# Performance work log

Measured on AMD Instinct MI355X. Metric: run time of the kernel, lower is better.

## Reference

```python
import jax, jax.numpy as jnp
import numpy as np

LMAX = 2
C = 128            # uniform multiplicity per degree
H = 128            # hidden channels
M = (LMAX + 1) ** 2  # 9 spherical coefficients
EPS = 1e-6


def _pack_indices():
    # flat layout per degree block: [mul, 2l+1] channel-major; packed layout: [coeff, channel]
    pack = np.zeros(M * C, dtype=np.int64)
    offset = 0
    for l in range(LMAX + 1):
        dim = 2 * l + 1
        for m in range(dim):
            coeff = l * l + m
            for c in range(C):
                pack[coeff * C + c] = offset + c * dim + m
        offset += C * dim
    unpack = np.argsort(pack)
    return jnp.asarray(pack), jnp.asarray(unpack)

PACK_IDX, UNPACK_IDX = _pack_indices()
# expand_index: degree index for each of the M coefficients
EXPAND_IDX = jnp.asarray(np.repeat(np.arange(LMAX + 1), 2 * np.arange(LMAX + 1) + 1))


def setup_inputs() -> dict:
    key = jax.random.key(0)
    ks = jax.random.split(key, 6)
    N = 10000
    A = 42  # (2*(lmax+1)) * (2*(lmax+1)+1) = 6*7 flattened S2 grid points
    bound = 1.0 / np.sqrt(C)
    return {
        "x": jax.random.normal(ks[0], (N, M * C), dtype=jnp.float32),
        "norm_weight": jnp.ones((LMAX + 1, C), dtype=jnp.float32),
        "w1": jax.random.uniform(ks[1], (LMAX + 1, H, C), jnp.float32, -bound, bound),
        "b1": jnp.zeros((1, 1, H), dtype=jnp.float32),
        "grid_w": jax.random.uniform(ks[2], (2 * H, H), jnp.float32, -bound, bound),
        "grid_b": jnp.zeros((2 * H,), dtype=jnp.float32),
        "w2": jax.random.uniform(ks[3], (LMAX + 1, C, H), jnp.float32, -bound, bound),
        "b2": jnp.zeros((1, 1, C), dtype=jnp.float32),
        "to_grid_mat": jax.random.normal(ks[4], (A, M), dtype=jnp.float32) * 0.3,
        "from_grid_mat": jax.random.normal(ks[5], (M, A), dtype=jnp.float32) * 0.3,
    }


def reference(x, norm_weight, w1, b1, grid_w, grid_b, w2, b2, to_grid_mat, from_grid_mat):
    N = x.shape[0]
    # --- pack flat irreps -> [N, M, C] (pure permutation gather; no padding for uniform irreps)
    p = jnp.take(x, PACK_IDX, axis=1).reshape(N, M, C)
    # --- merged equivariant RMS norm over all (coeff, channel), per-degree-channel affine
    rms = jnp.sqrt(jnp.mean(p * p, axis=(1, 2), keepdims=True) + EPS)
    h = (p / rms) * norm_weight[EXPAND_IDX][None]  # [N, M, C]
    # --- SO3LinearFlat #1: per-degree dense C -> H, bias only on l=0 coeff
    h = jnp.einsum("nmc,mhc->nmh", h, w1[EXPAND_IDX])
    h = h.at[:, 0:1, :].add(b1)
    # --- to S2 grid: [N, M, H] -> [N, A, H]
    g = jnp.einsum("am,nmh->nah", to_grid_mat, h)
    # --- pointwise SwiGLU on grid: H -> 2H linear, silu gate
    z = jnp.einsum("nah,oh->nao", g, grid_w) + grid_b
    g = jax.nn.silu(z[..., :H]) * z[..., H:]
    # --- from S2 grid: [N, A, H] -> [N, M, H]
    h = jnp.einsum("ma,nah->nmh", from_grid_mat, g)
    # --- SO3LinearFlat #2: per-degree dense H -> C, bias only on l=0 coeff
    out = jnp.einsum("nmh,mch->nmc", h, w2[EXPAND_IDX])
    out = out.at[:, 0:1, :].add(b2)
    # --- unpack back to flat irreps layout
    return jnp.take(out.reshape(N, M * C), UNPACK_IDX, axis=1)
```

## Files before the change

kernel.cpp:

```cpp
#include <hip/hip_runtime.h>
#include <math.h>

typedef unsigned short u16;
typedef __attribute__((ext_vector_type(8))) short bf16x8;
typedef __attribute__((ext_vector_type(4))) float f32x4;
typedef __attribute__((ext_vector_type(16))) float f32x16;

constexpr int OFF_W1 = 0;
constexpr int OFF_W2 = 49152;
constexpr int OFF_GW = 98304;
constexpr int OFF_TG = 131072;
constexpr int OFF_FG = 132096;
constexpr int WS_ELEMS = 134144;

__device__ __forceinline__ u16 f2bf(float f) {
    unsigned u = __float_as_uint(f);
    u += 0x7FFFu + ((u >> 16) & 1u);
    return (u16)(u >> 16);
}

__global__ void prep_kernel(const float* __restrict__ w1, const float* __restrict__ gw,
                            const float* __restrict__ w2, const float* __restrict__ tg,
                            const float* __restrict__ fg, u16* __restrict__ wsb) {
    const int idx = blockIdx.x * blockDim.x + threadIdx.x;
    const int str = gridDim.x * blockDim.x;
    for (int i = idx; i < 49152; i += str) wsb[OFF_W1 + i] = f2bf(w1[i]);
    for (int i = idx; i < 49152; i += str) wsb[OFF_W2 + i] = f2bf(w2[i]);
    for (int i = idx; i < 32768; i += str) wsb[OFF_GW + i] = f2bf(gw[i]);
    for (int i = idx; i < 1024; i += str) {
        int a = i >> 4, k = i & 15;
        wsb[OFF_TG + i] = (a < 42 && k < 9) ? f2bf(tg[a * 9 + k]) : (u16)0;
    }
    for (int i = idx; i < 2048; i += str) {
        int m = i >> 6, k = i & 63;
        wsb[OFF_FG + i] = (m < 9 && k < 42) ? f2bf(fg[m * 42 + k]) : (u16)0;
    }
}

__global__ __launch_bounds__(256, 2) void eqffn_mfma(
    const float* __restrict__ x, const float* __restrict__ nw,
    const float* __restrict__ b1f, const float* __restrict__ gbf,
    const float* __restrict__ b2f, const u16* __restrict__ wsb,
    float* __restrict__ out, int N)
{
    __shared__ u16 sh_a1[64 * 136];
    __shared__ u16 sh_h1T[4 * 128 * 16];
    __shared__ u16 sh_g[48 * 136];
    __shared__ u16 sh_g2T[128 * 72];
    __shared__ float sh_nw[384];
    __shared__ float sh_b1[128];
    __shared__ float sh_b2[128];
    __shared__ float sh_gb[256];

    const int tid  = threadIdx.x;
    const int w    = tid >> 6;
    const int lane = tid & 63;
    const int q    = lane >> 4;
    const int r    = lane & 15;
    const int r32  = lane & 31;
    const int half = lane >> 5;
    const int n0   = blockIdx.x * 4;

    for (int i = tid; i < 384; i += 256) sh_nw[i] = nw[i];
    if (tid < 128) { sh_b1[tid] = b1f[tid]; sh_b2[tid] = b2f[tid]; }
    sh_gb[tid] = gbf[tid];
    {
        unsigned long long* z1 = (unsigned long long*)sh_h1T;
        for (int i = tid; i < 2048; i += 256) z1[i] = 0ull;
        unsigned long long* z2 = (unsigned long long*)sh_g2T;
        for (int i = tid; i < 2304; i += 256) z2[i] = 0ull;
    }
    __syncthreads();

    const int myn = n0 + w;
    float4 xv[5];
    float ss = 0.f;
    if (myn < N) {
        const float4* xr = (const float4*)(x + (size_t)myn * 1152);
        for (int i = lane, c2 = 0; i < 288; i += 64, ++c2) {
            float4 v = xr[i]; xv[c2] = v;
            ss += v.x * v.x + v.y * v.y + v.z * v.z + v.w * v.w;
        }
    }
    #pragma unroll
    for (int off = 32; off; off >>= 1) ss += __shfl_xor(ss, off);
    const float inv = 1.0f / sqrtf(ss * (1.0f / 1152.0f) + 1e-6f);
    if (myn < N) {
        for (int i = lane, c2 = 0; i < 288; i += 64, ++c2) {
            float4 v = xv[c2];
            #pragma unroll
            for (int e = 0; e < 4; ++e) {
                const int f = i * 4 + e;
                const float val = ((const float*)&v)[e] * inv;
                int row, c, l;
                if (f < 128)      { l = 0; c = f;            row = w; }
                else if (f < 512) { int t = f - 128; l = 1; c = t / 3; row = 16 + w * 3 + (t - c * 3); }
                else              { int t = f - 512; l = 2; c = t / 5; row = 32 + w * 5 + (t - c * 5); }
                sh_a1[row * 136 + c] = f2bf(val * sh_nw[l * 128 + c]);
            }
        }
    }
    __syncthreads();

    {
        f32x4 acc[4][2];
        #pragma unroll
        for (int a = 0; a < 4; ++a)
            #pragma unroll
            for (int b = 0; b < 2; ++b)
                #pragma unroll
                for (int e = 0; e < 4; ++e) acc[a][b][e] = 0.f;
        #pragma unroll
        for (int mt = 0; mt < 4; ++mt) {
            const int l = (mt == 0) ? 0 : ((mt == 1) ? 1 : 2);
            #pragma unroll
            for (int k = 0; k < 4; ++k) {
                bf16x8 af = *(const bf16x8*)&sh_a1[(mt * 16 + r) * 136 + k * 32 + q * 8];
                #pragma unroll
                for (int nt = 0; nt < 2; ++nt) {
                    const int h = (2 * w + nt) * 16 + r;
                    bf16x8 bf = *(const bf16x8*)&wsb[OFF_W1 + (l * 128 + h) * 128 + k * 32 + q * 8];
                    acc[mt][nt] = __builtin_amdgcn_mfma_f32_16x16x32_bf16(af, bf, acc[mt][nt], 0, 0, 0);
                }
            }
        }
        #pragma unroll
        for (int mt = 0; mt < 4; ++mt) {
            #pragma unroll
            for (int nt = 0; nt < 2; ++nt) {
                const int h = (2 * w + nt) * 16 + r;
                #pragma unroll
                for (int rg = 0; rg < 4; ++rg) {
                    const int rr = q * 4 + rg;
                    const float v = acc[mt][nt][rg];
                    if (mt == 0) {
                        if (rr < 4) sh_h1T[(rr * 128 + h) * 16 + 0] = f2bf(v + sh_b1[h]);
                    } else if (mt == 1) {
                        if (rr < 12) { int nd = rr / 3, mm = rr - nd * 3; sh_h1T[(nd * 128 + h) * 16 + 1 + mm] = f2bf(v); }
                    } else {
                        int rr2 = (mt - 2) * 16 + rr;
                        if (rr2 < 20) { int nd = rr2 / 5, mm = rr2 - nd * 5; sh_h1T[(nd * 128 + h) * 16 + 4 + mm] = f2bf(v); }
                    }
                }
            }
        }
    }
    __syncthreads();

    for (int nn = 0; nn < 4; ++nn) {
        {
            bf16x8 bfr = *(const bf16x8*)&sh_h1T[(nn * 128 + w * 32 + r32) * 16 + half * 8];
            bf16x8 a0  = *(const bf16x8*)&wsb[OFF_TG + r32 * 16 + half * 8];
            bf16x8 a1  = *(const bf16x8*)&wsb[OFF_TG + (32 + r32) * 16 + half * 8];
            f32x16 ac0, ac1;
            #pragma unroll
            for (int e = 0; e < 16; ++e) { ac0[e] = 0.f; ac1[e] = 0.f; }
            ac0 = __builtin_amdgcn_mfma_f32_32x32x16_bf16(a0, bfr, ac0, 0, 0, 0);
            ac1 = __builtin_amdgcn_mfma_f32_32x32x16_bf16(a1, bfr, ac1, 0, 0, 0);
            const int h = w * 32 + r32;
            #pragma unroll
            for (int rg = 0; rg < 16; ++rg) {
                const int ar = (rg & 3) + 8 * (rg >> 2) + 4 * half;
                sh_g[ar * 136 + h] = f2bf(ac0[rg]);
                const int ar1 = 32 + ar;
                if (ar1 < 48) sh_g[ar1 * 136 + h] = f2bf(ac1[rg]);
            }
        }
        __syncthreads();

        {
            bf16x8 bfr[3][4];
            #pragma unroll
            for (int nt = 0; nt < 3; ++nt)
                #pragma unroll
                for (int k = 0; k < 4; ++k)
                    bfr[nt][k] = *(const bf16x8*)&sh_g[(nt * 16 + r) * 136 + k * 32 + q * 8];
            f32x4 aL[2][3], aH[2][3];
            #pragma unroll
            for (int p = 0; p < 2; ++p)
                #pragma unroll
                for (int nt = 0; nt < 3; ++nt)
                    #pragma unroll
                    for (int e = 0; e < 4; ++e) { aL[p][nt][e] = 0.f; aH[p][nt][e] = 0.f; }
            #pragma unroll
            for (int p = 0; p < 2; ++p) {
                const int oL = (2 * w + p) * 16 + r;
                const int oH = oL + 128;
                #pragma unroll
                for (int k = 0; k < 4; ++k) {
                    bf16x8 fL = *(const bf16x8*)&wsb[OFF_GW + oL * 128 + k * 32 + q * 8];
                    bf16x8 fH = *(const bf16x8*)&wsb[OFF_GW + oH * 128 + k * 32 + q * 8];
                    #pragma unroll
                    for (int nt = 0; nt < 3; ++nt) {
                        aL[p][nt] = __builtin_amdgcn_mfma_f32_16x16x32_bf16(fL, bfr[nt][k], aL[p][nt], 0, 0, 0);
                        aH[p][nt] = __builtin_amdgcn_mfma_f32_16x16x32_bf16(fH, bfr[nt][k], aH[p][nt], 0, 0, 0);
                    }
                }
            }
            #pragma unroll
            for (int p = 0; p < 2; ++p) {
                #pragma unroll
                for (int nt = 0; nt < 3; ++nt) {
                    #pragma unroll
                    for (int rg = 0; rg < 4; ++rg) {
                        const int o = (2 * w + p) * 16 + q * 4 + rg;
                        const int a = nt * 16 + r;
                        const float zl = aL[p][nt][rg] + sh_gb[o];
                        const float zh = aH[p][nt][rg] + sh_gb[128 + o];
                        const float gv = zl * (1.0f / (1.0f + __expf(-zl))) * zh;
                        if (a < 42) sh_g2T[o * 72 + a] = f2bf(gv);
                    }
                }
            }
        }
        __syncthreads();

        {
            f32x16 ac;
            #pragma unroll
            for (int e = 0; e < 16; ++e) ac[e] = 0.f;
            const int h = w * 32 + r32;
            #pragma unroll
            for (int k = 0; k < 4; ++k) {
                bf16x8 af = *(const bf16x8*)&wsb[OFF_FG + r32 * 64 + k * 16 + half * 8];
                bf16x8 bf = *(const bf16x8*)&sh_g2T[h * 72 + k * 16 + half * 8];
                ac = __builtin_amdgcn_mfma_f32_32x32x16_bf16(af, bf, ac, 0, 0, 0);
            }
            #pragma unroll
            for (int rg = 0; rg < 16; ++rg) {
                const int m = (rg & 3) + 8 * (rg >> 2) + 4 * half;
                if (m < 9) {
                    const int row = (m == 0) ? nn : ((m < 4) ? (16 + nn * 3 + (m - 1)) : (32 + nn * 5 + (m - 4)));
                    sh_a1[row * 136 + h] = f2bf(ac[rg]);
                }
            }
        }
    }
    __syncthreads();

    {
        f32x4 acc[4][2];
        #pragma unroll
        for (int a = 0; a < 4; ++a)
            #pragma unroll
            for (int b = 0; b < 2; ++b)
                #pragma unroll
                for (int e = 0; e < 4; ++e) acc[a][b][e] = 0.f;
        #pragma unroll
        for (int mt = 0; mt < 4; ++mt) {
            const int l = (mt == 0) ? 0 : ((mt == 1) ? 1 : 2);
            #pragma unroll
            for (int k = 0; k < 4; ++k) {
                bf16x8 af = *(const bf16x8*)&sh_a1[(mt * 16 + r) * 136 + k * 32 + q * 8];
                #pragma unroll
                for (int nt = 0; nt < 2; ++nt) {
                    const int c = (2 * w + nt) * 16 + r;
                    bf16x8 bf = *(const bf16x8*)&wsb[OFF_W2 + (l * 128 + c) * 128 + k * 32 + q * 8];
                    acc[mt][nt] = __builtin_amdgcn_mfma_f32_16x16x32_bf16(af, bf, acc[mt][nt], 0, 0, 0);
                }
            }
        }
        #pragma unroll
        for (int mt = 0; mt < 4; ++mt) {
            #pragma unroll
            for (int nt = 0; nt < 2; ++nt) {
                const int c = (2 * w + nt) * 16 + r;
                #pragma unroll
                for (int rg = 0; rg < 4; ++rg) {
                    const int rr = q * 4 + rg;
                    const float v = acc[mt][nt][rg];
                    if (mt == 0) {
                        if (rr < 4) { int gn = n0 + rr; if (gn < N) out[(size_t)gn * 1152 + c] = v + sh_b2[c]; }
                    } else if (mt == 1) {
                        if (rr < 12) { int nd = rr / 3, mm = rr - nd * 3; int gn = n0 + nd;
                                       if (gn < N) out[(size_t)gn * 1152 + 128 + c * 3 + mm] = v; }
                    } else {
                        int rr2 = (mt - 2) * 16 + rr;
                        if (rr2 < 20) { int nd = rr2 / 5, mm = rr2 - nd * 5; int gn = n0 + nd;
                                        if (gn < N) out[(size_t)gn * 1152 + 512 + c * 5 + mm] = v; }
                    }
                }
            }
        }
    }
}

extern "C" void kernel_launch(void* const* d_in, const int* in_sizes, int n_in,
                              void* d_out, int out_size, void* d_ws, size_t ws_size,
                              hipStream_t stream)
{
    const float* x  = (const float*)d_in[0];
    const float* nw = (const float*)d_in[1];
    const float* w1 = (const float*)d_in[2];
    const float* b1 = (const float*)d_in[3];
    const float* gw = (const float*)d_in[4];
    const float* gb = (const float*)d_in[5];
    const float* w2 = (const float*)d_in[6];
    const float* b2 = (const float*)d_in[7];
    const float* tg = (const float*)d_in[8];
    const float* fg = (const float*)d_in[9];
    float* out = (float*)d_out;
    u16* wsb = (u16*)d_ws;

    const int N = in_sizes[0] / 1152;
    prep_kernel<<<64, 256, 0, stream>>>(w1, gw, w2, tg, fg, wsb);
    eqffn_mfma<<<(N + 3) / 4, 256, 0, stream>>>(x, nw, b1, gb, b2, wsb, out, N);
}
```

Before: 256.9 us.

## Restructure grid transforms as node-expanded 16x16 MFMAs with staged coalesced output

Precomputes node-expanded to-grid and from-grid matrices so each node's grid transform becomes a 16x16x32 MFMA over the packed row layout. The from-grid results accumulate in registers across all four nodes instead of being scattered into shared memory each iteration. Shared buffers are aliased in a single pool, and intermediate results are written with packed 4-wide bf16 stores rather than scalar scatters. The final output is staged in shared memory and written as coalesced float4 rows instead of strided scalar global stores. The cost is extra zero-padded MFMA work in the expanded grid matrices and an added sync before the output pass.

```diff
diff --git a/kernel.cpp b/kernel.cpp
--- a/kernel.cpp
+++ b/kernel.cpp
@@ -4,19 +4,36 @@
 typedef unsigned short u16;
 typedef __attribute__((ext_vector_type(8))) short bf16x8;
 typedef __attribute__((ext_vector_type(4))) float f32x4;
-typedef __attribute__((ext_vector_type(16))) float f32x16;
-
-constexpr int OFF_W1 = 0;
-constexpr int OFF_W2 = 49152;
-constexpr int OFF_GW = 98304;
-constexpr int OFF_TG = 131072;
-constexpr int OFF_FG = 132096;
-constexpr int WS_ELEMS = 134144;
+
+constexpr int OFF_W1  = 0;
+constexpr int OFF_W2  = 49152;
+constexpr int OFF_GW  = 98304;
+constexpr int OFF_TGE = 131072;
+constexpr int OFF_FGE = 143360;
+
+constexpr int P_A1  = 0;
+constexpr int P_H1T = 17408;
+constexpr int P_G   = 35840;
+constexpr int P_G2T = 48896;
+constexpr int P_OUT = 17408;
+constexpr int P_SZ  = 67328;
 
 __device__ __forceinline__ u16 f2bf(float f) {
     unsigned u = __float_as_uint(f);
     u += 0x7FFFu + ((u >> 16) & 1u);
     return (u16)(u >> 16);
+}
+__device__ __forceinline__ void st4bf(void* p, f32x4 v) {
+    union { unsigned long long u; unsigned int w[2]; } d;
+    d.w[0] = (unsigned)f2bf(v[0]) | ((unsigned)f2bf(v[1]) << 16);
+    d.w[1] = (unsigned)f2bf(v[2]) | ((unsigned)f2bf(v[3]) << 16);
+    *(unsigned long long*)p = d.u;
+}
+__device__ __forceinline__ bool rowmap(int rp, int& n, int& m) {
+    if (rp < 4)              { n = rp; m = 0; return true; }
+    if (rp >= 16 && rp < 28) { int t = rp - 16; n = t / 3; m = 1 + t % 3; return true; }
+    if (rp >= 32 && rp < 52) { int t = rp - 32; n = t / 5; m = 4 + t % 5; return true; }
+    return false;
 }
 
 __global__ void prep_kernel(const float* __restrict__ w1, const float* __restrict__ gw,
@@ -27,49 +44,58 @@
     for (int i = idx; i < 49152; i += str) wsb[OFF_W1 + i] = f2bf(w1[i]);
     for (int i = idx; i < 49152; i += str) wsb[OFF_W2 + i] = f2bf(w2[i]);
     for (int i = idx; i < 32768; i += str) wsb[OFF_GW + i] = f2bf(gw[i]);
-    for (int i = idx; i < 1024; i += str) {
-        int a = i >> 4, k = i & 15;
-        wsb[OFF_TG + i] = (a < 42 && k < 9) ? f2bf(tg[a * 9 + k]) : (u16)0;
-    }
-    for (int i = idx; i < 2048; i += str) {
-        int m = i >> 6, k = i & 63;
-        wsb[OFF_FG + i] = (m < 9 && k < 42) ? f2bf(fg[m * 42 + k]) : (u16)0;
-    }
-}
-
-__global__ __launch_bounds__(256, 2) void eqffn_mfma(
-    const float* __restrict__ x, const float* __restrict__ nw,
+    for (int i = idx; i < 12288; i += str) {
+        int n = i / 3072, rem = i - n * 3072, a = rem >> 6, rp = rem & 63;
+        int nn, m; float v = 0.f;
+        if (a < 42 && rowmap(rp, nn, m) && nn == n) v = tg[a * 9 + m];
+        wsb[OFF_TGE + i] = f2bf(v);
+    }
+    for (int i = idx; i < 16384; i += str) {
+        int n = i >> 12, rem = i & 4095, rp = rem >> 6, a = rem & 63;
+        int nn, m; float v = 0.f;
+        if (a < 42 && rowmap(rp, nn, m) && nn == n) v = fg[m * 42 + a];
+        wsb[OFF_FGE + i] = f2bf(v);
+    }
+}
+
+#define MFMA16(A, B, C) __builtin_amdgcn_mfma_f32_16x16x32_bf16(A, B, C, 0, 0, 0)
+
+__global__ __launch_bounds__(256, 2) void eqffn2(
+    const float* __restrict__ x, const float* __restrict__ nwf,
     const float* __restrict__ b1f, const float* __restrict__ gbf,
     const float* __restrict__ b2f, const u16* __restrict__ wsb,
     float* __restrict__ out, int N)
 {
-    __shared__ u16 sh_a1[64 * 136];
-    __shared__ u16 sh_h1T[4 * 128 * 16];
-    __shared__ u16 sh_g[48 * 136];
-    __shared__ u16 sh_g2T[128 * 72];
+    __shared__ __align__(16) unsigned char pool[P_SZ];
     __shared__ float sh_nw[384];
     __shared__ float sh_b1[128];
     __shared__ float sh_b2[128];
     __shared__ float sh_gb[256];
+
+    u16*   A1  = (u16*)(pool + P_A1);
+    u16*   H1T = (u16*)(pool + P_H1T);
+    u16*   Gm  = (u16*)(pool + P_G);
+    u16*   G2T = (u16*)(pool + P_G2T);
+    float* OUTS = (float*)(pool + P_OUT);
 
     const int tid  = threadIdx.x;
     const int w    = tid >> 6;
     const int lane = tid & 63;
     const int q    = lane >> 4;
     const int r    = lane & 15;
-    const int r32  = lane & 31;
-    const int half = lane >> 5;
     const int n0   = blockIdx.x * 4;
 
-    for (int i = tid; i < 384; i += 256) sh_nw[i] = nw[i];
+    {
+        unsigned long long* z = (unsigned long long*)A1;
+        for (int i = tid; i < 2176; i += 256) z[i] = 0ull;
+        for (int i = tid; i < 512; i += 256) {
+            int h = i >> 2, p = i & 3;
+            *(unsigned long long*)(pool + P_G2T + h * 144 + 96 + p * 8) = 0ull;
+        }
+    }
+    for (int i = tid; i < 384; i += 256) sh_nw[i] = nwf[i];
     if (tid < 128) { sh_b1[tid] = b1f[tid]; sh_b2[tid] = b2f[tid]; }
     sh_gb[tid] = gbf[tid];
-    {
-        unsigned long long* z1 = (unsigned long long*)sh_h1T;
-        for (int i = tid; i < 2048; i += 256) z1[i] = 0ull;
-        unsigned long long* z2 = (unsigned long long*)sh_g2T;
-        for (int i = tid; i < 2304; i += 256) z2[i] = 0ull;
-    }
     __syncthreads();
 
     const int myn = n0 + w;
@@ -96,7 +122,7 @@
                 if (f < 128)      { l = 0; c = f;            row = w; }
                 else if (f < 512) { int t = f - 128; l = 1; c = t / 3; row = 16 + w * 3 + (t - c * 3); }
                 else              { int t = f - 512; l = 2; c = t / 5; row = 32 + w * 5 + (t - c * 5); }
-                sh_a1[row * 136 + c] = f2bf(val * sh_nw[l * 128 + c]);
+                A1[row * 136 + c] = f2bf(val * sh_nw[l * 128 + c]);
             }
         }
     }
@@ -114,172 +140,216 @@
         for (int mt = 0; mt < 4; ++mt) {
             const int l = (mt == 0) ? 0 : ((mt == 1) ? 1 : 2);
             #pragma unroll
-            for (int k = 0; k < 4; ++k) {
-                bf16x8 af = *(const bf16x8*)&sh_a1[(mt * 16 + r) * 136 + k * 32 + q * 8];
+            for (int kk = 0; kk < 4; ++kk) {
+                bf16x8 af = *(const bf16x8*)&A1[(mt * 16 + r) * 136 + kk * 32 + q * 8];
                 #pragma unroll
                 for (int nt = 0; nt < 2; ++nt) {
                     const int h = (2 * w + nt) * 16 + r;
-                    bf16x8 bf = *(const bf16x8*)&wsb[OFF_W1 + (l * 128 + h) * 128 + k * 32 + q * 8];
-                    acc[mt][nt] = __builtin_amdgcn_mfma_f32_16x16x32_bf16(af, bf, acc[mt][nt], 0, 0, 0);
-                }
-            }
-        }
-        #pragma unroll
-        for (int mt = 0; mt < 4; ++mt) {
-            #pragma unroll
-            for (int nt = 0; nt < 2; ++nt) {
-                const int h = (2 * w + nt) * 16 + r;
-                #pragma unroll
-                for (int rg = 0; rg < 4; ++rg) {
-                    const int rr = q * 4 + rg;
-                    const float v = acc[mt][nt][rg];
-                    if (mt == 0) {
-                        if (rr < 4) sh_h1T[(rr * 128 + h) * 16 + 0] = f2bf(v + sh_b1[h]);
-                    } else if (mt == 1) {
-                        if (rr < 12) { int nd = rr / 3, mm = rr - nd * 3; sh_h1T[(nd * 128 + h) * 16 + 1 + mm] = f2bf(v); }
-                    } else {
-                        int rr2 = (mt - 2) * 16 + rr;
-                        if (rr2 < 20) { int nd = rr2 / 5, mm = rr2 - nd * 5; sh_h1T[(nd * 128 + h) * 16 + 4 + mm] = f2bf(v); }
+                    bf16x8 bf = *(const bf16x8*)&wsb[OFF_W1 + (l * 128 + h) * 128 + kk * 32 + q * 8];
+                    acc[mt][nt] = MFMA16(af, bf, acc[mt][nt]);
+                }
+            }
+        }
+        #pragma unroll
+        for (int nt = 0; nt < 2; ++nt) {
+            const int h = (2 * w + nt) * 16 + r;
+            const float bias = sh_b1[h];
+            #pragma unroll
+            for (int mt = 0; mt < 4; ++mt) {
+                f32x4 v = acc[mt][nt];
+                if (mt == 0) {
+                    #pragma unroll
+                    for (int e = 0; e < 4; ++e) v[e] += bias;
+                }
+                st4bf(&H1T[h * 72 + mt * 16 + q * 4], v);
+            }
+        }
+    }
+    __syncthreads();
+
+    float gbL[2], gbH[2];
+    #pragma unroll
+    for (int p = 0; p < 2; ++p) {
+        const int oL = (2 * w + p) * 16 + r;
+        gbL[p] = sh_gb[oL]; gbH[p] = sh_gb[128 + oL];
+    }
+
+    f32x4 afg[2][4];
+    #pragma unroll
+    for (int a = 0; a < 2; ++a)
+        #pragma unroll
+        for (int b = 0; b < 4; ++b)
+            #pragma unroll
+            for (int e = 0; e < 4; ++e) afg[a][b][e] = 0.f;
+
+    for (int n = 0; n < 4; ++n) {
+        {
+            const u16* TGn = wsb + OFF_TGE + n * 3072;
+            f32x4 ac[2][3];
+            #pragma unroll
+            for (int a = 0; a < 2; ++a)
+                #pragma unroll
+                for (int b = 0; b < 3; ++b)
+                    #pragma unroll
+                    for (int e = 0; e < 4; ++e) ac[a][b][e] = 0.f;
+            #pragma unroll
+            for (int kk = 0; kk < 2; ++kk) {
+                bf16x8 af[2];
+                #pragma unroll
+                for (int Mt = 0; Mt < 2; ++Mt)
+                    af[Mt] = *(const bf16x8*)&H1T[((2 * w + Mt) * 16 + r) * 72 + kk * 32 + q * 8];
+                #pragma unroll
+                for (int nt = 0; nt < 3; ++nt) {
+                    bf16x8 bf = *(const bf16x8*)&TGn[(nt * 16 + r) * 64 + kk * 32 + q * 8];
+                    #pragma unroll
+                    for (int Mt = 0; Mt < 2; ++Mt) ac[Mt][nt] = MFMA16(af[Mt], bf, ac[Mt][nt]);
+                }
+            }
+            #pragma unroll
+            for (int nt = 0; nt < 3; ++nt)
+                #pragma unroll
+                for (int Mt = 0; Mt < 2; ++Mt)
+                    st4bf(&Gm[(nt * 16 + r) * 136 + (2 * w + Mt) * 16 + q * 4], ac[Mt][nt]);
+        }
+        __syncthreads();
+
+        {
+            f32x4 aL[2][3], aH[2][3];
+            #pragma unroll
+            for (int p = 0; p < 2; ++p)
+                #pragma unroll
+                for (int Mt = 0; Mt < 3; ++Mt)
+                    #pragma unroll
+                    for (int e = 0; e < 4; ++e) { aL[p][Mt][e] = 0.f; aH[p][Mt][e] = 0.f; }
+            #pragma unroll
+            for (int kk = 0; kk < 4; ++kk) {
+                bf16x8 ga[3];
+                #pragma unroll
+                for (int Mt = 0; Mt < 3; ++Mt)
+                    ga[Mt] = *(const bf16x8*)&Gm[(Mt * 16 + r) * 136 + kk * 32 + q * 8];
+                #pragma unroll
+                for (int p = 0; p < 2; ++p) {
+                    const int oL = (2 * w + p) * 16 + r;
+                    bf16x8 bL = *(const bf16x8*)&wsb[OFF_GW + oL * 128 + kk * 32 + q * 8];
+                    bf16x8 bH = *(const bf16x8*)&wsb[OFF_GW + (oL + 128) * 128 + kk * 32 + q * 8];
+                    #pragma unroll
+                    for (int Mt = 0; Mt < 3; ++Mt) {
+                        aL[p][Mt] = MFMA16(ga[Mt], bL, aL[p][Mt]);
+                        aH[p][Mt] = MFMA16(ga[Mt], bH, aH[p][Mt]);
                     }
                 }
             }
-        }
-    }
-    __syncthreads();
-
-    for (int nn = 0; nn < 4; ++nn) {
-        {
-            bf16x8 bfr = *(const bf16x8*)&sh_h1T[(nn * 128 + w * 32 + r32) * 16 + half * 8];
-            bf16x8 a0  = *(const bf16x8*)&wsb[OFF_TG + r32 * 16 + half * 8];
-            bf16x8 a1  = *(const bf16x8*)&wsb[OFF_TG + (32 + r32) * 16 + half * 8];
-            f32x16 ac0, ac1;
-            #pragma unroll
-            for (int e = 0; e < 16; ++e) { ac0[e] = 0.f; ac1[e] = 0.f; }
-            ac0 = __builtin_amdgcn_mfma_f32_32x32x16_bf16(a0, bfr, ac0, 0, 0, 0);
-            ac1 = __builtin_amdgcn_mfma_f32_32x32x16_bf16(a1, bfr, ac1, 0, 0, 0);
-            const int h = w * 32 + r32;
-            #pragma unroll
-            for (int rg = 0; rg < 16; ++rg) {
-                const int ar = (rg & 3) + 8 * (rg >> 2) + 4 * half;
-                sh_g[ar * 136 + h] = f2bf(ac0[rg]);
-                const int ar1 = 32 + ar;
-                if (ar1 < 48) sh_g[ar1 * 136 + h] = f2bf(ac1[rg]);
-            }
-        }
-        __syncthreads();
-
-        {
-            bf16x8 bfr[3][4];
-            #pragma unroll
-            for (int nt = 0; nt < 3; ++nt)
-                #pragma unroll
-                for (int k = 0; k < 4; ++k)
-                    bfr[nt][k] = *(const bf16x8*)&sh_g[(nt * 16 + r) * 136 + k * 32 + q * 8];
-            f32x4 aL[2][3], aH[2][3];
-            #pragma unroll
-            for (int p = 0; p < 2; ++p)
-                #pragma unroll
-                for (int nt = 0; nt < 3; ++nt)
-                    #pragma unroll
-                    for (int e = 0; e < 4; ++e) { aL[p][nt][e] = 0.f; aH[p][nt][e] = 0.f; }
             #pragma unroll
             for (int p = 0; p < 2; ++p) {
                 const int oL = (2 * w + p) * 16 + r;
-                const int oH = oL + 128;
-                #pragma unroll
-                for (int k = 0; k < 4; ++k) {
-                    bf16x8 fL = *(const bf16x8*)&wsb[OFF_GW + oL * 128 + k * 32 + q * 8];
-                    bf16x8 fH = *(const bf16x8*)&wsb[OFF_GW + oH * 128 + k * 32 + q * 8];
-                    #pragma unroll
-                    for (int nt = 0; nt < 3; ++nt) {
-                        aL[p][nt] = __builtin_amdgcn_mfma_f32_16x16x32_bf16(fL, bfr[nt][k], aL[p][nt], 0, 0, 0);
-                        aH[p][nt] = __builtin_amdgcn_mfma_f32_16x16x32_bf16(fH, bfr[nt][k], aH[p][nt], 0, 0, 0);
+                #pragma unroll
+                for (int Mt = 0; Mt < 3; ++Mt) {
+                    f32x4 g;
+                    #pragma unroll
+                    for (int e = 0; e < 4; ++e) {
+                        const float zl = aL[p][Mt][e] + gbL[p];
+                        const float zh = aH[p][Mt][e] + gbH[p];
+                        g[e] = zl * (1.0f / (1.0f + __expf(-zl))) * zh;
                     }
-                }
-            }
-            #pragma unroll
-            for (int p = 0; p < 2; ++p) {
-                #pragma unroll
-                for (int nt = 0; nt < 3; ++nt) {
-                    #pragma unroll
-                    for (int rg = 0; rg < 4; ++rg) {
-                        const int o = (2 * w + p) * 16 + q * 4 + rg;
-                        const int a = nt * 16 + r;
-                        const float zl = aL[p][nt][rg] + sh_gb[o];
-                        const float zh = aH[p][nt][rg] + sh_gb[128 + o];
-                        const float gv = zl * (1.0f / (1.0f + __expf(-zl))) * zh;
-                        if (a < 42) sh_g2T[o * 72 + a] = f2bf(gv);
+                    st4bf(&G2T[oL * 72 + Mt * 16 + q * 4], g);
+                }
+            }
+        }
+        __syncthreads();
+
+        {
+            const u16* FGn = wsb + OFF_FGE + n * 4096;
+            #pragma unroll
+            for (int kk = 0; kk < 2; ++kk) {
+                bf16x8 af[2];
+                #pragma unroll
+                for (int Mt = 0; Mt < 2; ++Mt)
+                    af[Mt] = *(const bf16x8*)&G2T[((2 * w + Mt) * 16 + r) * 72 + kk * 32 + q * 8];
+                #pragma unroll
+                for (int nt = 0; nt < 4; ++nt) {
+                    bf16x8 bf = *(const bf16x8*)&FGn[(nt * 16 + r) * 64 + kk * 32 + q * 8];
+                    #pragma unroll
+                    for (int Mt = 0; Mt < 2; ++Mt) afg[Mt][nt] = MFMA16(af[Mt], bf, afg[Mt][nt]);
+                }
+            }
+        }
+    }
+
+    #pragma unroll
+    for (int nt = 0; nt < 4; ++nt)
+        #pragma unroll
+        for (int Mt = 0; Mt < 2; ++Mt)
+            st4bf(&A1[(nt * 16 + r) * 136 + (2 * w + Mt) * 16 + q * 4], afg[Mt][nt]);
+    __syncthreads();
+
+    {
+        f32x4 ac[2][4];
+        #pragma unroll
+        for (int a = 0; a < 2; ++a)
+            #pragma unroll
+            for (int b = 0; b < 4; ++b)
+                #pragma unroll
+                for (int e = 0; e < 4; ++e) ac[a][b][e] = 0.f;
+        #pragma unroll
+        for (int kk = 0; kk < 4; ++kk) {
+            bf16x8 bh[4];
+            #pragma unroll
+            for (int nt = 0; nt < 4; ++nt)
+                bh[nt] = *(const bf16x8*)&A1[(nt * 16 + r) * 136 + kk * 32 + q * 8];
+            #pragma unroll
+            for (int Mt = 0; Mt < 2; ++Mt) {
+                const int c = (2 * w + Mt) * 16 + r;
+                bf16x8 a0 = *(const bf16x8*)&wsb[OFF_W2 + (0 * 128 + c) * 128 + kk * 32 + q * 8];
+                bf16x8 a1 = *(const bf16x8*)&wsb[OFF_W2 + (1 * 128 + c) * 128 + kk * 32 + q * 8];
+                bf16x8 a2 = *(const bf16x8*)&wsb[OFF_W2 + (2 * 128 + c) * 128 + kk * 32 + q * 8];
+                ac[Mt][0] = MFMA16(a0, bh[0], ac[Mt][0]);
+                ac[Mt][1] = MFMA16(a1, bh[1], ac[Mt][1]);
+                ac[Mt][2] = MFMA16(a2, bh[2], ac[Mt][2]);
+                ac[Mt][3] = MFMA16(a2, bh[3], ac[Mt][3]);
+            }
+        }
+        #pragma unroll
+        for (int Mt = 0; Mt < 2; ++Mt) {
+            const int cb = (2 * w + Mt) * 16 + q * 4;
+            const float4 bias = *(const float4*)&sh_b2[cb];
+            #pragma unroll
+            for (int nt = 0; nt < 4; ++nt) {
+                const int rp = nt * 16 + r;
+                f32x4 v = ac[Mt][nt];
+                if (nt == 0 && r < 4) {
+                    v[0] += bias.x; v[1] += bias.y; v[2] += bias.z; v[3] += bias.w;
+                }
+                *(float4*)&OUTS[rp * 132 + cb] = *(float4*)&v;
+            }
+        }
+    }
+    __syncthreads();
+
+    {
+        const int nloc = tid >> 6;
+        const int gn = n0 + nloc;
+        if (gn < N) {
+            float4* orow = (float4*)(out + (size_t)gn * 1152);
+            for (int j = lane; j < 288; j += 64) {
+                float4 v;
+                if (j < 32) {
+                    v = *(const float4*)&OUTS[nloc * 132 + j * 4];
+                } else if (j < 128) {
+                    const int t = j * 4 - 128;
+                    #pragma unroll
+                    for (int e = 0; e < 4; ++e) {
+                        const int te = t + e, c = te / 3, mm = te - 3 * c;
+                        ((float*)&v)[e] = OUTS[(16 + nloc * 3 + mm) * 132 + c];
                     }
-                }
-            }
-        }
-        __syncthreads();
-
-        {
-            f32x16 ac;
-            #pragma unroll
-            for (int e = 0; e < 16; ++e) ac[e] = 0.f;
-            const int h = w * 32 + r32;
-            #pragma unroll
-            for (int k = 0; k < 4; ++k) {
-                bf16x8 af = *(const bf16x8*)&wsb[OFF_FG + r32 * 64 + k * 16 + half * 8];
-                bf16x8 bf = *(const bf16x8*)&sh_g2T[h * 72 + k * 16 + half * 8];
-                ac = __builtin_amdgcn_mfma_f32_32x32x16_bf16(af, bf, ac, 0, 0, 0);
-            }
-            #pragma unroll
-            for (int rg = 0; rg < 16; ++rg) {
-                const int m = (rg & 3) + 8 * (rg >> 2) + 4 * half;
-                if (m < 9) {
-                    const int row = (m == 0) ? nn : ((m < 4) ? (16 + nn * 3 + (m - 1)) : (32 + nn * 5 + (m - 4)));
-                    sh_a1[row * 136 + h] = f2bf(ac[rg]);
-                }
-            }
-        }
-    }
-    __syncthreads();
-
-    {
-        f32x4 acc[4][2];
-        #pragma unroll
-        for (int a = 0; a < 4; ++a)
-            #pragma unroll
-            for (int b = 0; b < 2; ++b)
-                #pragma unroll
-                for (int e = 0; e < 4; ++e) acc[a][b][e] = 0.f;
-        #pragma unroll
-        for (int mt = 0; mt < 4; ++mt) {
-            const int l = (mt == 0) ? 0 : ((mt == 1) ? 1 : 2);
-            #pragma unroll
-            for (int k = 0; k < 4; ++k) {
-                bf16x8 af = *(const bf16x8*)&sh_a1[(mt * 16 + r) * 136 + k * 32 + q * 8];
-                #pragma unroll
-                for (int nt = 0; nt < 2; ++nt) {
-                    const int c = (2 * w + nt) * 16 + r;
-                    bf16x8 bf = *(const bf16x8*)&wsb[OFF_W2 + (l * 128 + c) * 128 + k * 32 + q * 8];
-                    acc[mt][nt] = __builtin_amdgcn_mfma_f32_16x16x32_bf16(af, bf, acc[mt][nt], 0, 0, 0);
-                }
-            }
-        }
-        #pragma unroll
-        for (int mt = 0; mt < 4; ++mt) {
-            #pragma unroll
-            for (int nt = 0; nt < 2; ++nt) {
-                const int c = (2 * w + nt) * 16 + r;
-                #pragma unroll
-                for (int rg = 0; rg < 4; ++rg) {
-                    const int rr = q * 4 + rg;
-                    const float v = acc[mt][nt][rg];
-                    if (mt == 0) {
-                        if (rr < 4) { int gn = n0 + rr; if (gn < N) out[(size_t)gn * 1152 + c] = v + sh_b2[c]; }
-                    } else if (mt == 1) {
-                        if (rr < 12) { int nd = rr / 3, mm = rr - nd * 3; int gn = n0 + nd;
-                                       if (gn < N) out[(size_t)gn * 1152 + 128 + c * 3 + mm] = v; }
-                    } else {
-                        int rr2 = (mt - 2) * 16 + rr;
-                        if (rr2 < 20) { int nd = rr2 / 5, mm = rr2 - nd * 5; int gn = n0 + nd;
-                                        if (gn < N) out[(size_t)gn * 1152 + 512 + c * 5 + mm] = v; }
+                } else {
+                    const int t = j * 4 - 512;
+                    #pragma unroll
+                    for (int e = 0; e < 4; ++e) {
+                        const int te = t + e, c = te / 5, mm = te - 5 * c;
+                        ((float*)&v)[e] = OUTS[(32 + nloc * 5 + mm) * 132 + c];
                     }
                 }
+                orow[j] = v;
             }
         }
     }
@@ -303,6 +373,6 @@
     u16* wsb = (u16*)d_ws;
 
     const int N = in_sizes[0] / 1152;
-    prep_kernel<<<64, 256, 0, stream>>>(w1, gw, w2, tg, fg, wsb);
-    eqffn_mfma<<<(N + 3) / 4, 256, 0, stream>>>(x, nw, b1, gb, b2, wsb, out, N);
-}
+    prep_kernel<<<128, 256, 0, stream>>>(w1, gw, w2, tg, fg, wsb);
+    eqffn2<<<(N + 3) / 4, 256, 0, stream>>>(x, nw, b1, gb, b2, wsb, out, N);
+}
```

Result: slower. 302.7 us (+17.8%).

## Process two nodes per block with tighter MFMA tiles and trimmed padding

Applied to the files above, without the earlier changes.

Each block now handles two nodes instead of four. This lets the per-degree linear layers use three 16-row M-tiles instead of four, and it cuts the grid-coefficient K padding from 64 to 48. The shared-memory footprint shrinks and launch bounds target 3 blocks per CU. Biases are held in registers and the SwiGLU output is stored as packed 4-wide bf16, with the loop order swapped so grid activations act as the A operand. In exchange, more blocks each reload the same weights from global/L2, so weight reuse per node is lower.

```diff
diff --git a/kernel.cpp b/kernel.cpp
--- a/kernel.cpp
+++ b/kernel.cpp
@@ -11,12 +11,17 @@
 constexpr int OFF_GW = 98304;
 constexpr int OFF_TG = 131072;
 constexpr int OFF_FG = 132096;
-constexpr int WS_ELEMS = 134144;
 
 __device__ __forceinline__ u16 f2bf(float f) {
     unsigned u = __float_as_uint(f);
     u += 0x7FFFu + ((u >> 16) & 1u);
     return (u16)(u >> 16);
+}
+__device__ __forceinline__ void st4bf(void* p, f32x4 v) {
+    union { unsigned long long u; unsigned int w[2]; } d;
+    d.w[0] = (unsigned)f2bf(v[0]) | ((unsigned)f2bf(v[1]) << 16);
+    d.w[1] = (unsigned)f2bf(v[2]) | ((unsigned)f2bf(v[3]) << 16);
+    *(unsigned long long*)p = d.u;
 }
 
 __global__ void prep_kernel(const float* __restrict__ w1, const float* __restrict__ gw,
@@ -28,29 +33,30 @@
     for (int i = idx; i < 49152; i += str) wsb[OFF_W2 + i] = f2bf(w2[i]);
     for (int i = idx; i < 32768; i += str) wsb[OFF_GW + i] = f2bf(gw[i]);
     for (int i = idx; i < 1024; i += str) {
-        int a = i >> 4, k = i & 15;
-        wsb[OFF_TG + i] = (a < 42 && k < 9) ? f2bf(tg[a * 9 + k]) : (u16)0;
-    }
-    for (int i = idx; i < 2048; i += str) {
-        int m = i >> 6, k = i & 63;
-        wsb[OFF_FG + i] = (m < 9 && k < 42) ? f2bf(fg[m * 42 + k]) : (u16)0;
-    }
-}
-
-__global__ __launch_bounds__(256, 2) void eqffn_mfma(
-    const float* __restrict__ x, const float* __restrict__ nw,
+        int a = i >> 4, m = i & 15;
+        wsb[OFF_TG + i] = (a < 42 && m < 9) ? f2bf(tg[a * 9 + m]) : (u16)0;
+    }
+    for (int i = idx; i < 1536; i += str) {
+        int m = i / 48, a = i - m * 48;
+        wsb[OFF_FG + i] = (m < 9 && a < 42) ? f2bf(fg[m * 42 + a]) : (u16)0;
+    }
+}
+
+#define MFMA16(A, B, C) __builtin_amdgcn_mfma_f32_16x16x32_bf16(A, B, C, 0, 0, 0)
+#define MFMA32(A, B, C) __builtin_amdgcn_mfma_f32_32x32x16_bf16(A, B, C, 0, 0, 0)
+
+__global__ __launch_bounds__(256, 3) void eqffn3(
+    const float* __restrict__ x, const float* __restrict__ nwf,
     const float* __restrict__ b1f, const float* __restrict__ gbf,
     const float* __restrict__ b2f, const u16* __restrict__ wsb,
     float* __restrict__ out, int N)
 {
-    __shared__ u16 sh_a1[64 * 136];
-    __shared__ u16 sh_h1T[4 * 128 * 16];
-    __shared__ u16 sh_g[48 * 136];
-    __shared__ u16 sh_g2T[128 * 72];
+    __shared__ __align__(16) u16 A1[48 * 136];
+    __shared__ __align__(16) u16 H1T[2 * 128 * 16];
+    __shared__ __align__(16) u16 Gg[48 * 136];
+    __shared__ __align__(16) u16 G2T[128 * 56];
     __shared__ float sh_nw[384];
-    __shared__ float sh_b1[128];
-    __shared__ float sh_b2[128];
-    __shared__ float sh_gb[256];
+    __shared__ float sh_red[4];
 
     const int tid  = threadIdx.x;
     const int w    = tid >> 6;
@@ -59,87 +65,101 @@
     const int r    = lane & 15;
     const int r32  = lane & 31;
     const int half = lane >> 5;
-    const int n0   = blockIdx.x * 4;
-
-    for (int i = tid; i < 384; i += 256) sh_nw[i] = nw[i];
-    if (tid < 128) { sh_b1[tid] = b1f[tid]; sh_b2[tid] = b2f[tid]; }
-    sh_gb[tid] = gbf[tid];
+    const int n0   = blockIdx.x * 2;
+
     {
-        unsigned long long* z1 = (unsigned long long*)sh_h1T;
-        for (int i = tid; i < 2048; i += 256) z1[i] = 0ull;
-        unsigned long long* z2 = (unsigned long long*)sh_g2T;
-        for (int i = tid; i < 2304; i += 256) z2[i] = 0ull;
+        unsigned long long* z = (unsigned long long*)H1T;
+        for (int i = tid; i < 1024; i += 256) z[i] = 0ull;
+    }
+    for (int i = tid; i < 384; i += 256) sh_nw[i] = nwf[i];
+
+    float b1v[2], b2v[2], gbL[2], gbH[2];
+    #pragma unroll
+    for (int t = 0; t < 2; ++t) {
+        const int col = w * 32 + t * 16 + r;
+        b1v[t] = b1f[col];
+        b2v[t] = b2f[col];
+        gbL[t] = gbf[col];
+        gbH[t] = gbf[128 + col];
     }
     __syncthreads();
 
-    const int myn = n0 + w;
-    float4 xv[5];
+    const int nd   = tid >> 7;
+    const int pl   = tid & 127;
+    const int myn  = n0 + nd;
+    const bool valid = (myn < N);
+    float4 xv[3];
+    int   nv = 0;
     float ss = 0.f;
-    if (myn < N) {
+    if (valid) {
         const float4* xr = (const float4*)(x + (size_t)myn * 1152);
-        for (int i = lane, c2 = 0; i < 288; i += 64, ++c2) {
-            float4 v = xr[i]; xv[c2] = v;
+        for (int i = pl; i < 288; i += 128, ++nv) {
+            float4 v = xr[i]; xv[nv] = v;
             ss += v.x * v.x + v.y * v.y + v.z * v.z + v.w * v.w;
         }
     }
     #pragma unroll
     for (int off = 32; off; off >>= 1) ss += __shfl_xor(ss, off);
-    const float inv = 1.0f / sqrtf(ss * (1.0f / 1152.0f) + 1e-6f);
-    if (myn < N) {
-        for (int i = lane, c2 = 0; i < 288; i += 64, ++c2) {
-            float4 v = xv[c2];
+    if (lane == 0) sh_red[w] = ss;
+    __syncthreads();
+    const float inv = 1.0f / sqrtf((sh_red[nd * 2] + sh_red[nd * 2 + 1]) * (1.0f / 1152.0f) + 1e-6f);
+
+    if (valid) {
+        for (int ii = 0, i = pl; ii < nv; ++ii, i += 128) {
+            float4 v = xv[ii];
             #pragma unroll
             for (int e = 0; e < 4; ++e) {
                 const int f = i * 4 + e;
                 const float val = ((const float*)&v)[e] * inv;
                 int row, c, l;
-                if (f < 128)      { l = 0; c = f;            row = w; }
-                else if (f < 512) { int t = f - 128; l = 1; c = t / 3; row = 16 + w * 3 + (t - c * 3); }
-                else              { int t = f - 512; l = 2; c = t / 5; row = 32 + w * 5 + (t - c * 5); }
-                sh_a1[row * 136 + c] = f2bf(val * sh_nw[l * 128 + c]);
+                if (f < 128)      { l = 0; c = f;                        row = nd; }
+                else if (f < 512) { int t = f - 128; l = 1; c = t / 3;   row = 16 + nd * 3 + (t - c * 3); }
+                else              { int t = f - 512; l = 2; c = t / 5;   row = 32 + nd * 5 + (t - c * 5); }
+                A1[row * 136 + c] = f2bf(val * sh_nw[l * 128 + c]);
             }
         }
     }
     __syncthreads();
 
     {
-        f32x4 acc[4][2];
-        #pragma unroll
-        for (int a = 0; a < 4; ++a)
+        f32x4 acc[3][2];
+        #pragma unroll
+        for (int a = 0; a < 3; ++a)
             #pragma unroll
             for (int b = 0; b < 2; ++b)
                 #pragma unroll
                 for (int e = 0; e < 4; ++e) acc[a][b][e] = 0.f;
         #pragma unroll
-        for (int mt = 0; mt < 4; ++mt) {
-            const int l = (mt == 0) ? 0 : ((mt == 1) ? 1 : 2);
-            #pragma unroll
-            for (int k = 0; k < 4; ++k) {
-                bf16x8 af = *(const bf16x8*)&sh_a1[(mt * 16 + r) * 136 + k * 32 + q * 8];
-                #pragma unroll
-                for (int nt = 0; nt < 2; ++nt) {
-                    const int h = (2 * w + nt) * 16 + r;
-                    bf16x8 bf = *(const bf16x8*)&wsb[OFF_W1 + (l * 128 + h) * 128 + k * 32 + q * 8];
-                    acc[mt][nt] = __builtin_amdgcn_mfma_f32_16x16x32_bf16(af, bf, acc[mt][nt], 0, 0, 0);
-                }
-            }
-        }
-        #pragma unroll
-        for (int mt = 0; mt < 4; ++mt) {
+        for (int kk = 0; kk < 4; ++kk) {
+            bf16x8 af[3];
+            #pragma unroll
+            for (int Mt = 0; Mt < 3; ++Mt)
+                af[Mt] = *(const bf16x8*)&A1[(Mt * 16 + r) * 136 + kk * 32 + q * 8];
             #pragma unroll
             for (int nt = 0; nt < 2; ++nt) {
-                const int h = (2 * w + nt) * 16 + r;
+                const int h = w * 32 + nt * 16 + r;
+                #pragma unroll
+                for (int Mt = 0; Mt < 3; ++Mt) {
+                    bf16x8 bf = *(const bf16x8*)&wsb[OFF_W1 + (Mt * 128 + h) * 128 + kk * 32 + q * 8];
+                    acc[Mt][nt] = MFMA16(af[Mt], bf, acc[Mt][nt]);
+                }
+            }
+        }
+        #pragma unroll
+        for (int nt = 0; nt < 2; ++nt) {
+            const int h = w * 32 + nt * 16 + r;
+            #pragma unroll
+            for (int Mt = 0; Mt < 3; ++Mt) {
                 #pragma unroll
                 for (int rg = 0; rg < 4; ++rg) {
                     const int rr = q * 4 + rg;
-                    const float v = acc[mt][nt][rg];
-                    if (mt == 0) {
-                        if (rr < 4) sh_h1T[(rr * 128 + h) * 16 + 0] = f2bf(v + sh_b1[h]);
-                    } else if (mt == 1) {
-                        if (rr < 12) { int nd = rr / 3, mm = rr - nd * 3; sh_h1T[(nd * 128 + h) * 16 + 1 + mm] = f2bf(v); }
+                    const float v = acc[Mt][nt][rg];
+                    if (Mt == 0) {
+                        if (rr < 2) H1T[rr * 2048 + h * 16 + 0] = f2bf(v + b1v[nt]);
+                    } else if (Mt == 1) {
+                        if (rr < 6) { int d = rr / 3, mm = rr - d * 3; H1T[d * 2048 + h * 16 + 1 + mm] = f2bf(v); }
                     } else {
-                        int rr2 = (mt - 2) * 16 + rr;
-                        if (rr2 < 20) { int nd = rr2 / 5, mm = rr2 - nd * 5; sh_h1T[(nd * 128 + h) * 16 + 4 + mm] = f2bf(v); }
+                        if (rr < 10) { int d = rr / 5, mm = rr - d * 5; H1T[d * 2048 + h * 16 + 4 + mm] = f2bf(v); }
                     }
                 }
             }
@@ -147,137 +167,135 @@
     }
     __syncthreads();
 
-    for (int nn = 0; nn < 4; ++nn) {
+    for (int n = 0; n < 2; ++n) {
         {
-            bf16x8 bfr = *(const bf16x8*)&sh_h1T[(nn * 128 + w * 32 + r32) * 16 + half * 8];
+            const int h = w * 32 + r32;
+            bf16x8 bfr = *(const bf16x8*)&H1T[n * 2048 + h * 16 + half * 8];
             bf16x8 a0  = *(const bf16x8*)&wsb[OFF_TG + r32 * 16 + half * 8];
             bf16x8 a1  = *(const bf16x8*)&wsb[OFF_TG + (32 + r32) * 16 + half * 8];
             f32x16 ac0, ac1;
             #pragma unroll
             for (int e = 0; e < 16; ++e) { ac0[e] = 0.f; ac1[e] = 0.f; }
-            ac0 = __builtin_amdgcn_mfma_f32_32x32x16_bf16(a0, bfr, ac0, 0, 0, 0);
-            ac1 = __builtin_amdgcn_mfma_f32_32x32x16_bf16(a1, bfr, ac1, 0, 0, 0);
-            const int h = w * 32 + r32;
+            ac0 = MFMA32(a0, bfr, ac0);
+            ac1 = MFMA32(a1, bfr, ac1);
             #pragma unroll
             for (int rg = 0; rg < 16; ++rg) {
                 const int ar = (rg & 3) + 8 * (rg >> 2) + 4 * half;
-                sh_g[ar * 136 + h] = f2bf(ac0[rg]);
-                const int ar1 = 32 + ar;
-                if (ar1 < 48) sh_g[ar1 * 136 + h] = f2bf(ac1[rg]);
+                Gg[ar * 136 + h] = f2bf(ac0[rg]);
+                if (ar < 16) Gg[(32 + ar) * 136 + h] = f2bf(ac1[rg]);
             }
         }
         __syncthreads();
 
         {
-            bf16x8 bfr[3][4];
-            #pragma unroll
-            for (int nt = 0; nt < 3; ++nt)
-                #pragma unroll
-                for (int k = 0; k < 4; ++k)
-                    bfr[nt][k] = *(const bf16x8*)&sh_g[(nt * 16 + r) * 136 + k * 32 + q * 8];
             f32x4 aL[2][3], aH[2][3];
             #pragma unroll
             for (int p = 0; p < 2; ++p)
                 #pragma unroll
-                for (int nt = 0; nt < 3; ++nt)
+                for (int Mt = 0; Mt < 3; ++Mt)
                     #pragma unroll
-                    for (int e = 0; e < 4; ++e) { aL[p][nt][e] = 0.f; aH[p][nt][e] = 0.f; }
+                    for (int e = 0; e < 4; ++e) { aL[p][Mt][e] = 0.f; aH[p][Mt][e] = 0.f; }
+            #pragma unroll
+            for (int kk = 0; kk < 4; ++kk) {
+                bf16x8 ga[3];
+                #pragma unroll
+                for (int Mt = 0; Mt < 3; ++Mt)
+                    ga[Mt] = *(const bf16x8*)&Gg[(Mt * 16 + r) * 136 + kk * 32 + q * 8];
+                #pragma unroll
+                for (int p = 0; p < 2; ++p) {
+                    const int oL = w * 32 + p * 16 + r;
+                    bf16x8 bL = *(const bf16x8*)&wsb[OFF_GW + oL * 128 + kk * 32 + q * 8];
+                    bf16x8 bH = *(const bf16x8*)&wsb[OFF_GW + (oL + 128) * 128 + kk * 32 + q * 8];
+                    #pragma unroll
+                    for (int Mt = 0; Mt < 3; ++Mt) {
+                        aL[p][Mt] = MFMA16(ga[Mt], bL, aL[p][Mt]);
+                        aH[p][Mt] = MFMA16(ga[Mt], bH, aH[p][Mt]);
+                    }
+                }
+            }
             #pragma unroll
             for (int p = 0; p < 2; ++p) {
-                const int oL = (2 * w + p) * 16 + r;
-                const int oH = oL + 128;
-                #pragma unroll
-                for (int k = 0; k < 4; ++k) {
-                    bf16x8 fL = *(const bf16x8*)&wsb[OFF_GW + oL * 128 + k * 32 + q * 8];
-                    bf16x8 fH = *(const bf16x8*)&wsb[OFF_GW + oH * 128 + k * 32 + q * 8];
+                const int oL = w * 32 + p * 16 + r;
+                #pragma unroll
+                for (int Mt = 0; Mt < 3; ++Mt) {
+                    f32x4 g;
                     #pragma unroll
-                    for (int nt = 0; nt < 3; ++nt) {
-                        aL[p][nt] = __builtin_amdgcn_mfma_f32_16x16x32_bf16(fL, bfr[nt][k], aL[p][nt], 0, 0, 0);
-                        aH[p][nt] = __builtin_amdgcn_mfma_f32_16x16x32_bf16(fH, bfr[nt][k], aH[p][nt], 0, 0, 0);
+                    for (int e = 0; e < 4; ++e) {
+                        const float zl = aL[p][Mt][e] + gbL[p];
+                        const float zh = aH[p][Mt][e] + gbH[p];
+                        g[e] = zl * (1.0f / (1.0f + __expf(-zl))) * zh;
                     }
-                }
-            }
-            #pragma unroll
-            for (int p = 0; p < 2; ++p) {
-                #pragma unroll
-                for (int nt = 0; nt < 3; ++nt) {
-                    #pragma unroll
-                    for (int rg = 0; rg < 4; ++rg) {
-                        const int o = (2 * w + p) * 16 + q * 4 + rg;
-                        const int a = nt * 16 + r;
-                        const float zl = aL[p][nt][rg] + sh_gb[o];
-                        const float zh = aH[p][nt][rg] + sh_gb[128 + o];
-                        const float gv = zl * (1.0f / (1.0f + __expf(-zl))) * zh;
-                        if (a < 42) sh_g2T[o * 72 + a] = f2bf(gv);
-                    }
+                    st4bf(&G2T[oL * 56 + Mt * 16 + q * 4], g);
                 }
             }
         }
         __syncthreads();
 
         {
+            const int h = w * 32 + r32;
             f32x16 ac;
             #pragma unroll
             for (int e = 0; e < 16; ++e) ac[e] = 0.f;
-            const int h = w * 32 + r32;
-            #pragma unroll
-            for (int k = 0; k < 4; ++k) {
-                bf16x8 af = *(const bf16x8*)&wsb[OFF_FG + r32 * 64 + k * 16 + half * 8];
-                bf16x8 bf = *(const bf16x8*)&sh_g2T[h * 72 + k * 16 + half * 8];
-                ac = __builtin_amdgcn_mfma_f32_32x32x16_bf16(af, bf, ac, 0, 0, 0);
+            #pragma unroll
+            for (int kk = 0; kk < 3; ++kk) {
+                bf16x8 af = *(const bf16x8*)&wsb[OFF_FG + r32 * 48 + kk * 16 + half * 8];
+                bf16x8 bf = *(const bf16x8*)&G2T[h * 56 + kk * 16 + half * 8];
+                ac = MFMA32(af, bf, ac);
             }
             #pragma unroll
             for (int rg = 0; rg < 16; ++rg) {
                 const int m = (rg & 3) + 8 * (rg >> 2) + 4 * half;
                 if (m < 9) {
-                    const int row = (m == 0) ? nn : ((m < 4) ? (16 + nn * 3 + (m - 1)) : (32 + nn * 5 + (m - 4)));
-                    sh_a1[row * 136 + h] = f2bf(ac[rg]);
-                }
-            }
-        }
-    }
-    __syncthreads();
+                    const int row = (m == 0) ? n : ((m < 4) ? (16 + n * 3 + m - 1) : (32 + n * 5 + m - 4));
+                    A1[row * 136 + h] = f2bf(ac[rg]);
+                }
+            }
+        }
+        __syncthreads();
+    }
 
     {
-        f32x4 acc[4][2];
-        #pragma unroll
-        for (int a = 0; a < 4; ++a)
+        f32x4 acc[3][2];
+        #pragma unroll
+        for (int a = 0; a < 3; ++a)
             #pragma unroll
             for (int b = 0; b < 2; ++b)
                 #pragma unroll
                 for (int e = 0; e < 4; ++e) acc[a][b][e] = 0.f;
         #pragma unroll
-        for (int mt = 0; mt < 4; ++mt) {
-            const int l = (mt == 0) ? 0 : ((mt == 1) ? 1 : 2);
-            #pragma unroll
-            for (int k = 0; k < 4; ++k) {
-                bf16x8 af = *(const bf16x8*)&sh_a1[(mt * 16 + r) * 136 + k * 32 + q * 8];
-                #pragma unroll
-                for (int nt = 0; nt < 2; ++nt) {
-                    const int c = (2 * w + nt) * 16 + r;
-                    bf16x8 bf = *(const bf16x8*)&wsb[OFF_W2 + (l * 128 + c) * 128 + k * 32 + q * 8];
-                    acc[mt][nt] = __builtin_amdgcn_mfma_f32_16x16x32_bf16(af, bf, acc[mt][nt], 0, 0, 0);
-                }
-            }
-        }
-        #pragma unroll
-        for (int mt = 0; mt < 4; ++mt) {
+        for (int kk = 0; kk < 4; ++kk) {
+            bf16x8 af[3];
+            #pragma unroll
+            for (int Mt = 0; Mt < 3; ++Mt)
+                af[Mt] = *(const bf16x8*)&A1[(Mt * 16 + r) * 136 + kk * 32 + q * 8];
             #pragma unroll
             for (int nt = 0; nt < 2; ++nt) {
-                const int c = (2 * w + nt) * 16 + r;
+                const int c = w * 32 + nt * 16 + r;
+                #pragma unroll
+                for (int Mt = 0; Mt < 3; ++Mt) {
+                    bf16x8 bf = *(const bf16x8*)&wsb[OFF_W2 + (Mt * 128 + c) * 128 + kk * 32 + q * 8];
+                    acc[Mt][nt] = MFMA16(af[Mt], bf, acc[Mt][nt]);
+                }
+            }
+        }
+        #pragma unroll
+        for (int nt = 0; nt < 2; ++nt) {
+            const int c = w * 32 + nt * 16 + r;
+            #pragma unroll
+            for (int Mt = 0; Mt < 3; ++Mt) {
                 #pragma unroll
                 for (int rg = 0; rg < 4; ++rg) {
                     const int rr = q * 4 + rg;
-                    const float v = acc[mt][nt][rg];
-                    if (mt == 0) {
-                        if (rr < 4) { int gn = n0 + rr; if (gn < N) out[(size_t)gn * 1152 + c] = v + sh_b2[c]; }
-                    } else if (mt == 1) {
-                        if (rr < 12) { int nd = rr / 3, mm = rr - nd * 3; int gn = n0 + nd;
-                                       if (gn < N) out[(size_t)gn * 1152 + 128 + c * 3 + mm] = v; }
+                    const float v = acc[Mt][nt][rg];
+                    if (Mt == 0) {
+                        if (rr < 2) { int gn = n0 + rr;
+                            if (gn < N) out[(size_t)gn * 1152 + c] = v + b2v[nt]; }
+                    } else if (Mt == 1) {
+                        if (rr < 6) { int d = rr / 3, mm = rr - d * 3; int gn = n0 + d;
+                            if (gn < N) out[(size_t)gn * 1152 + 128 + c * 3 + mm] = v; }
                     } else {
-                        int rr2 = (mt - 2) * 16 + rr;
-                        if (rr2 < 20) { int nd = rr2 / 5, mm = rr2 - nd * 5; int gn = n0 + nd;
-                                        if (gn < N) out[(size_t)gn * 1152 + 512 + c * 5 + mm] = v; }
+                        if (rr < 10) { int d = rr / 5, mm = rr - d * 5; int gn = n0 + d;
+                            if (gn < N) out[(size_t)gn * 1152 + 512 + c * 5 + mm] = v; }
                     }
                 }
             }
@@ -303,6 +321,6 @@
     u16* wsb = (u16*)d_ws;
 
     const int N = in_sizes[0] / 1152;
-    prep_kernel<<<64, 256, 0, stream>>>(w1, gw, w2, tg, fg, wsb);
-    eqffn_mfma<<<(N + 3) / 4, 256, 0, stream>>>(x, nw, b1, gb, b2, wsb, out, N);
-}
+    prep_kernel<<<128, 256, 0, stream>>>(w1, gw, w2, tg, fg, wsb);
+    eqffn3<<<(N + 1) / 2, 256, 0, stream>>>(x, nw, b1, gb, b2, wsb, out, N);
+}
```

Result: slower. 331.6 us (+29.1%).
